# Optimization experiments

Measured on AMD Instinct MI355X. Metric: run time of the kernel, lower is better.

## Reference

```python
import jax, jax.numpy as jnp
import numpy as np
from jax import lax

DIM = 1024
H = 16          # num_heads
HD = DIM // H   # head dim (qk and v identical)
D_INNER = 4     # fast-weight inner dim
CHUNK = 16
BASE_LR = 1e-3
KSZ = 4         # short conv kernel size


def short_conv(x, w):
    # x: (b, l, c), w: (c, KSZ). Depthwise causal conv + residual (as in ShortConvolution).
    xT = jnp.transpose(x, (0, 2, 1))  # (b, c, l)
    y = lax.conv_general_dilated(xT, w[:, None, :], window_strides=(1,),
                                 padding=[(KSZ - 1, 0)], feature_group_count=x.shape[-1],
                                 dimension_numbers=('NCH', 'OIH', 'NCH'))
    return jnp.transpose(y + xT, (0, 2, 1))


def l2norm(x):
    # interpret torch.norm(..., dim=-1) as L2 normalization over head dim (required for shape consistency)
    return x / jnp.linalg.norm(x, axis=-1, keepdims=True)


def attn(q, k, v):
    # flash_attn_func equivalent: non-causal softmax attention, scale 1/sqrt(d)
    # q: (b, D, h, d), k/v: (b, L, h, d)
    s = jnp.einsum('bqhd,bkhd->bhqk', q, k) / jnp.sqrt(jnp.asarray(q.shape[-1], q.dtype))
    p = jax.nn.softmax(s, axis=-1)
    return jnp.einsum('bhqk,bkhd->bqhd', p, v)


def setup_inputs() -> dict:
    key = jax.random.key(0)
    ks = jax.random.split(key, 12)
    b, l = 4, 4096
    s = 1.0 / np.sqrt(DIM)
    return {
        'hidden_states': jax.random.normal(ks[0], (b, l, DIM), jnp.float32),
        'Wq': jax.random.normal(ks[1], (DIM, DIM), jnp.float32) * s,
        'Wk': jax.random.normal(ks[2], (DIM, DIM), jnp.float32) * s,
        'Wv': jax.random.normal(ks[3], (DIM, DIM), jnp.float32) * s,
        'Wlr': jax.random.normal(ks[4], (H * 2, DIM), jnp.float32) * s,
        'Wg': jax.random.normal(ks[5], (DIM, DIM), jnp.float32) * s,
        'Wo': jax.random.normal(ks[6], (DIM, DIM), jnp.float32) * s,
        'cq': jax.random.normal(ks[7], (DIM, KSZ), jnp.float32) * 0.1,
        'ck': jax.random.normal(ks[8], (DIM, KSZ), jnp.float32) * 0.1,
        'cv': jax.random.normal(ks[9], (DIM, KSZ), jnp.float32) * 0.1,
        'W_in_init': jax.random.normal(ks[10], (1, D_INNER, H, HD), jnp.float32) / np.sqrt(HD),
        'W_out_init': jax.random.normal(ks[11], (1, D_INNER, H, HD), jnp.float32) / np.sqrt(D_INNER),
        'ln_g': jnp.ones((HD,), jnp.float32),
        'ln_b': jnp.zeros((HD,), jnp.float32),
    }


def _forward(hidden_states, Wq, Wk, Wv, Wlr, Wg, Wo, cq, ck, cv, W_in_init, W_out_init, ln_g, ln_b):
    b, l, _ = hidden_states.shape
    q = l2norm(jax.nn.silu(short_conv(hidden_states @ Wq.T, cq)).reshape(b, l, H, HD))
    k = l2norm(jax.nn.silu(short_conv(hidden_states @ Wk.T, ck)).reshape(b, l, H, HD))
    v = jax.nn.silu(short_conv(hidden_states @ Wv.T, cv)).reshape(b, l, H, HD)
    lr = jax.nn.softplus(hidden_states @ Wlr.T + BASE_LR).reshape(b, l, H, 2)

    nc = l // CHUNK
    to_chunks = lambda x: x.reshape(b, nc, CHUNK, H, -1).transpose(1, 0, 2, 3, 4)
    qc, kc, vc, lrc = map(to_chunks, (q, k, v, lr))

    W_in0 = jnp.broadcast_to(W_in_init, (b, D_INNER, H, HD))
    W_out0 = jnp.broadcast_to(W_out_init, (b, D_INNER, H, HD))
    mask = jnp.tril(jnp.ones((CHUNK, CHUNK), jnp.float32))  # causal within chunk (diag kept)

    def step(carry, xs):
        W_in, W_out = carry
        q_t, k_t, v_t, lr_t = xs  # (b, CHUNK, H, d) / lr (b, CHUNK, H, 2)
        k_h = jax.nn.softmax(jnp.einsum('blhd,bDhd->blhD', k_t, W_in), axis=-1) * lr_t[..., 1:]
        q_h = jax.nn.softmax(jnp.einsum('blhd,bDhd->blhD', q_t, W_in), axis=-1)
        qk = jnp.einsum('bqhD,bkhD->bhqk', q_h, k_h) * mask
        o_t = jnp.einsum('bqhD,bDhd->bqhd', q_h, W_out) + jnp.einsum('bhqk,bkhd->bqhd', qk, v_t)
        W_out = W_out + jnp.einsum('bnhD,bnhd->bDhd', k_h, v_t)
        lr_in = lr_t[:, :1, :, 0:1]    # (b,1,h,1)
        lr_out = lr_t[:, :1, :, 1:2]
        # two nested test-time gradient steps via attention
        for _ in range(2):
            g_out = -attn(W_in, k_t, v_t)
            g_in = -attn(W_out, v_t, k_t)
            W_in = W_in - lr_in * g_in
            W_out = W_out - lr_out * g_out
        return (W_in, W_out), o_t

    _, o = lax.scan(step, (W_in0, W_out0), (qc, kc, vc, lrc))
    o = o.transpose(1, 0, 2, 3, 4).reshape(b, l, H, HD)

    mu = o.mean(-1, keepdims=True)
    var = ((o - mu) ** 2).mean(-1, keepdims=True)
    o = (o - mu) / jnp.sqrt(var + 1e-5) * ln_g + ln_b
    o = o.reshape(b, l, DIM)
    gate = hidden_states @ Wg.T
    return (o * gate) @ Wo.T


def reference(hidden_states, Wq, Wk, Wv, Wlr, Wg, Wo, cq, ck, cv, W_in_init, W_out_init, ln_g, ln_b):
    return _forward(hidden_states, Wq, Wk, Wv, Wlr, Wg, Wo, cq, ck, cv, W_in_init, W_out_init, ln_g, ln_b)
```

## Files before the change

### kernel.cpp

```cpp
#include <hip/hip_runtime.h>
#include <cstdint>
#include <cstddef>

#define DIM    1024
#define NH     16
#define HD     64
#define CHUNK_ 16
#define SEQ    4096
#define BATCH  4
#define NROWS  (BATCH * SEQ)
#define NCHUNK (SEQ / CHUNK_)
#define SEG    64
#define NSEG   (SEQ / SEG)

using bf16x8 = __attribute__((ext_vector_type(8))) short;
using f32x4  = __attribute__((ext_vector_type(4))) float;
typedef union { bf16x8 v; uint32_t u[4]; } B8;

#define MFMA16(a, b, c) __builtin_amdgcn_mfma_f32_16x16x32_bf16((a), (b), (c), 0, 0, 0)

__device__ __forceinline__ ushort f2bf(float f) {
    uint32_t u = __float_as_uint(f);
    u += 0x7FFFu + ((u >> 16) & 1u);
    return (ushort)(u >> 16);
}
__device__ __forceinline__ uint32_t pack2(float a, float b) {
    return (uint32_t)f2bf(a) | ((uint32_t)f2bf(b) << 16);
}
__device__ __forceinline__ float dot4(const float4 a, const float4 b) {
    return a.x*b.x + a.y*b.y + a.z*b.z + a.w*b.w;
}

template <int N>
__device__ __forceinline__ float ror16(float x) {
    return __int_as_float(__builtin_amdgcn_update_dpp(
        0, __float_as_int(x), 0x120 + N, 0xF, 0xF, true));
}
__device__ __forceinline__ float dppsum16(float x) {
    x += ror16<1>(x); x += ror16<2>(x);
    x += ror16<4>(x); x += ror16<8>(x);
    return x;
}

#define SYNC() do { asm volatile("" ::: "memory");          \
                    __builtin_amdgcn_wave_barrier();        \
                    __builtin_amdgcn_sched_barrier(0); } while (0)

__global__ __launch_bounds__(256)
void gemm_nt_bf16(const float* __restrict__ A, const float* __restrict__ B,
                  float* __restrict__ C, int K, int ldc)
{
    __shared__ ushort As[128][64];
    __shared__ ushort Bs[128][64];

    const int tid  = threadIdx.x;
    const int m0   = blockIdx.y * 128, n0 = blockIdx.x * 128;
    const int wave = tid >> 6, lane = tid & 63;
    const int wm   = (wave >> 1) * 64, wn = (wave & 1) * 64;
    const int frow = lane & 15, fkg = lane >> 4;
    const int srow = tid >> 1, shalf = tid & 1;

    f32x4 acc[4][4];
#pragma unroll
    for (int i = 0; i < 4; ++i)
#pragma unroll
        for (int j = 0; j < 4; ++j) acc[i][j] = (f32x4){0.f, 0.f, 0.f, 0.f};

    const float* Ap0 = A + (size_t)(m0 + srow) * K + shalf * 16;
    const float* Bp0 = B + (size_t)(n0 + srow) * K + shalf * 16;
    const int swz0 = ((shalf * 2 + 0) ^ (srow & 7)) * 8;
    const int swz1 = ((shalf * 2 + 1) ^ (srow & 7)) * 8;
    const int rsw  = (frow & 7);

    for (int kt = 0; kt < K; kt += 32) {
        float4 a0 = *(const float4*)(Ap0 + kt);
        float4 a1 = *(const float4*)(Ap0 + kt + 4);
        float4 a2 = *(const float4*)(Ap0 + kt + 8);
        float4 a3 = *(const float4*)(Ap0 + kt + 12);
        float4 b0 = *(const float4*)(Bp0 + kt);
        float4 b1 = *(const float4*)(Bp0 + kt + 4);
        float4 b2 = *(const float4*)(Bp0 + kt + 8);
        float4 b3 = *(const float4*)(Bp0 + kt + 12);

        __syncthreads();
        uint4 u;
        u.x = pack2(a0.x, a0.y); u.y = pack2(a0.z, a0.w);
        u.z = pack2(a1.x, a1.y); u.w = pack2(a1.z, a1.w);
        *(uint4*)&As[srow][swz0] = u;
        u.x = pack2(a2.x, a2.y); u.y = pack2(a2.z, a2.w);
        u.z = pack2(a3.x, a3.y); u.w = pack2(a3.z, a3.w);
        *(uint4*)&As[srow][swz1] = u;
        u.x = pack2(b0.x, b0.y); u.y = pack2(b0.z, b0.w);
        u.z = pack2(b1.x, b1.y); u.w = pack2(b1.z, b1.w);
        *(uint4*)&Bs[srow][swz0] = u;
        u.x = pack2(b2.x, b2.y); u.y = pack2(b2.z, b2.w);
        u.z = pack2(b3.x, b3.y); u.w = pack2(b3.z, b3.w);
        *(uint4*)&Bs[srow][swz1] = u;
        __syncthreads();

        bf16x8 af[4], bf[4];
#pragma unroll
        for (int i = 0; i < 4; ++i) {
            af[i] = *(const bf16x8*)&As[wm + i * 16 + frow][(fkg ^ rsw) * 8];
            bf[i] = *(const bf16x8*)&Bs[wn + i * 16 + frow][(fkg ^ rsw) * 8];
        }
#pragma unroll
        for (int mt = 0; mt < 4; ++mt)
#pragma unroll
            for (int nt = 0; nt < 4; ++nt)
                acc[mt][nt] = MFMA16(af[mt], bf[nt], acc[mt][nt]);
    }

    const int col = lane & 15, r4 = (lane >> 4) * 4;
#pragma unroll
    for (int mt = 0; mt < 4; ++mt)
#pragma unroll
        for (int nt = 0; nt < 4; ++nt)
#pragma unroll
            for (int j = 0; j < 4; ++j)
                C[(size_t)(m0 + wm + mt * 16 + r4 + j) * ldc +
                  (n0 + wn + nt * 16 + col)] = acc[mt][nt][j];
}

__global__ __launch_bounds__(256)
void lr_kernel(const float* __restrict__ hs, const float* __restrict__ Wlr,
               float* __restrict__ LR)
{
    __shared__ float row[DIM];
    const int r = blockIdx.x;
    const int t = threadIdx.x;
    *(float4*)&row[t * 4] = *(const float4*)&hs[(size_t)r * DIM + t * 4];
    __syncthreads();

    const int o = t >> 3;
    const int p = t & 7;
    const float* w = Wlr + (size_t)o * DIM + p * 128;
    const float* x = row + p * 128;
    float acc = 0.f;
#pragma unroll
    for (int i = 0; i < 32; ++i) {
        float4 xv = *(const float4*)(x + i * 4);
        float4 wv = *(const float4*)(w + i * 4);
        acc += dot4(xv, wv);
    }
    acc += __shfl_xor(acc, 1);
    acc += __shfl_xor(acc, 2);
    acc += __shfl_xor(acc, 4);
    if (p == 0) {
        float xx = acc + 0.001f;
        LR[(size_t)r * 32 + o] = (xx > 20.f) ? xx : log1pf(expf(xx));
    }
}

__global__ __launch_bounds__(256)
void halo_save(const float* __restrict__ Q, const float* __restrict__ K,
               const float* __restrict__ V, float* __restrict__ HALO)
{
    int idx = blockIdx.x;
    int tn  = idx / (BATCH * (NSEG - 1) * 3);
    int rem = idx - tn * (BATCH * (NSEG - 1) * 3);
    int b   = rem / ((NSEG - 1) * 3);
    int rem2= rem - b * ((NSEG - 1) * 3);
    int s   = rem2 / 3 + 1;
    int j   = rem2 - (s - 1) * 3;

    const float* buf = (tn == 0) ? Q : ((tn == 1) ? K : V);
    size_t src = ((size_t)(b * SEQ + s * SEG - 3 + j)) * DIM + threadIdx.x * 4;
    size_t dst = ((size_t)((tn * BATCH + b) * NSEG + s) * 3 + j) * DIM + threadIdx.x * 4;
    *(float4*)&HALO[dst] = *(const float4*)&buf[src];
}

__global__ __launch_bounds__(256)
void conv_inplace(float* __restrict__ Q, float* __restrict__ K,
                  float* __restrict__ V, const float* __restrict__ HALO,
                  const float* __restrict__ cq, const float* __restrict__ ck,
                  const float* __restrict__ cv)
{
    const int wid  = (blockIdx.x << 2) + (threadIdx.x >> 6);
    const int lane = threadIdx.x & 63;
    const int tn   = wid >> 12;
    const int rem  = wid & 4095;
    const int b    = rem >> 10;
    const int rem2 = rem & 1023;
    const int h    = rem2 >> 6;
    const int s    = rem2 & 63;
    const int c    = (h << 6) + lane;

    float* buf = (tn == 0) ? Q : ((tn == 1) ? K : V);
    const float* cw = (tn == 0) ? cq : ((tn == 1) ? ck : cv);
    float4 w4 = *(const float4*)(cw + (c << 2));

    float xm3 = 0.f, xm2 = 0.f, xm1 = 0.f;
    if (s > 0) {
        size_t hb = ((size_t)((tn * BATCH + b) * NSEG + s) * 3) * DIM + c;
        xm3 = HALO[hb];
        xm2 = HALO[hb + DIM];
        xm1 = HALO[hb + 2 * DIM];
    }

    size_t base = ((size_t)(b * SEQ + s * SEG)) * DIM + c;
    float x_next = buf[base];
#pragma unroll 4
    for (int i = 0; i < SEG; ++i) {
        float x = x_next;
        if (i < SEG - 1) x_next = buf[base + (size_t)(i + 1) * DIM];
        float y = xm3 * w4.x + xm2 * w4.y + xm1 * w4.z + x * w4.w + x;
        y = y / (1.f + __expf(-y));
        if (tn < 2) {
            float n2 = y * y;
#pragma unroll
            for (int m = 1; m < 64; m <<= 1) n2 += __shfl_xor(n2, m);
            y *= rsqrtf(n2);
        }
        buf[base + (size_t)i * DIM] = y;
        xm3 = xm2; xm2 = xm1; xm1 = x;
    }
}

__global__ __launch_bounds__(64)
void scan_kernel(const float* QP, const float* __restrict__ KP,
                 const float* __restrict__ VP, const float* __restrict__ LRb,
                 const float* __restrict__ GATE,
                 const float* __restrict__ Wi0, const float* __restrict__ Wo0,
                 const float* __restrict__ lng, const float* __restrict__ lnb,
                 float* OB)
{
    const int bh = blockIdx.x, b = bh >> 4, h = bh & 15;
    const int t  = threadIdx.x, lo = t & 15, g = t >> 4;

    __shared__ ushort KA[16][72], QA[16][72], VA[16][72];
    __shared__ ushort KT[64][24];
    __shared__ ushort VT[64][40];
    __shared__ ushort WiA[16][72], WoA[16][72];
    __shared__ ushort QKT[16][32];
    __shared__ ushort KH[16][32];
    __shared__ float  sG[16][68];

    for (int i = t; i < 16 * 72; i += 64) { ((ushort*)WiA)[i] = 0; ((ushort*)WoA)[i] = 0; }
    for (int i = t; i < 64 * 24; i += 64) ((ushort*)KT)[i] = 0;
    for (int i = t; i < 64 * 40; i += 64) ((ushort*)VT)[i] = 0;
    for (int i = t; i < 16 * 32; i += 64) { ((ushort*)QKT)[i] = 0; ((ushort*)KH)[i] = 0; }

    f32x4 wiC[4], woC[4];
#pragma unroll
    for (int n = 0; n < 4; ++n) { wiC[n] = (f32x4){0,0,0,0}; woC[n] = (f32x4){0,0,0,0}; }
    if (g == 0) {
#pragma unroll
        for (int n = 0; n < 4; ++n)
#pragma unroll
            for (int D = 0; D < 4; ++D) {
                float wi = Wi0[((size_t)D * NH + h) * HD + 16 * n + lo];
                float wo = Wo0[((size_t)D * NH + h) * HD + 16 * n + lo];
                wiC[n][D] = wi; woC[n][D] = wo;
                WiA[D][16 * n + lo] = f2bf(wi);
                WoA[D][16 * n + lo] = f2bf(wo);
                VT[16 * n + lo][16 + D] = f2bf(wo);
            }
    }
    SYNC();

    float lnGr[4], lnBr[4];
#pragma unroll
    for (int n = 0; n < 4; ++n) { lnGr[n] = lng[16 * n + lo]; lnBr[n] = lnb[16 * n + lo]; }

    const int rowb = b * SEQ;
    float4 pq[4], pk[4], pv[4], pg[4];
    float plr_q, plr_i, plr_o;
    {
#pragma unroll
        for (int i = 0; i < 4; ++i) {
            size_t go = (size_t)(rowb + i * 4 + g) * DIM + h * 64 + 4 * lo;
            pq[i] = *(const float4*)&QP[go];
            pk[i] = *(const float4*)&KP[go];
            pv[i] = *(const float4*)&VP[go];
            pg[i] = *(const float4*)&GATE[go];
        }
        plr_q = LRb[(size_t)(rowb + lo) * 32 + h * 2 + 1];
        plr_i = LRb[(size_t)rowb * 32 + h * 2];
        plr_o = LRb[(size_t)rowb * 32 + h * 2 + 1];
    }

    const f32x4 z4 = (f32x4){0.f, 0.f, 0.f, 0.f};
    const uint32_t pmsk = (g < 2) ? 0xFFFFFFFFu : 0u;
    const int L0 = (lo + 32 * g) & 63, L1 = (L0 + 16) & 63;

    for (int c = 0; c < NCHUNK; ++c) {
        const int rb = rowb + c * CHUNK_;

#pragma unroll
        for (int i = 0; i < 4; ++i) {
            const int row = i * 4 + g;
            *(float4*)&sG[row][4 * lo] = pg[i];
            uint2 uq; uq.x = pack2(pq[i].x, pq[i].y); uq.y = pack2(pq[i].z, pq[i].w);
            *(uint2*)&QA[row][4 * lo] = uq;
            uint2 uk; uk.x = pack2(pk[i].x, pk[i].y); uk.y = pack2(pk[i].z, pk[i].w);
            *(uint2*)&KA[row][4 * lo] = uk;
            uint2 uv; uv.x = pack2(pv[i].x, pv[i].y); uv.y = pack2(pv[i].z, pv[i].w);
            *(uint2*)&VA[row][4 * lo] = uv;
            KT[4 * lo + 0][row] = (ushort)(uk.x & 0xFFFF);
            KT[4 * lo + 1][row] = (ushort)(uk.x >> 16);
            KT[4 * lo + 2][row] = (ushort)(uk.y & 0xFFFF);
            KT[4 * lo + 3][row] = (ushort)(uk.y >> 16);
            VT[4 * lo + 0][row] = (ushort)(uv.x & 0xFFFF);
            VT[4 * lo + 1][row] = (ushort)(uv.x >> 16);
            VT[4 * lo + 2][row] = (ushort)(uv.y & 0xFFFF);
            VT[4 * lo + 3][row] = (ushort)(uv.y >> 16);
        }
        const float lr1    = plr_q;
        const float lr_in  = plr_i;
        const float lr_out = plr_o;

        if (c + 1 < NCHUNK) {
            const int rb2 = rb + CHUNK_;
#pragma unroll
            for (int i = 0; i < 4; ++i) {
                size_t go = (size_t)(rb2 + i * 4 + g) * DIM + h * 64 + 4 * lo;
                pq[i] = *(const float4*)&QP[go];
                pk[i] = *(const float4*)&KP[go];
                pv[i] = *(const float4*)&VP[go];
                pg[i] = *(const float4*)&GATE[go];
            }
            plr_q = LRb[(size_t)(rb2 + lo) * 32 + h * 2 + 1];
            plr_i = LRb[(size_t)rb2 * 32 + h * 2];
            plr_o = LRb[(size_t)rb2 * 32 + h * 2 + 1];
        }
        SYNC();

        bf16x8 xWi0 = *(const bf16x8*)&WiA[lo][g * 8];
        bf16x8 xWi1 = *(const bf16x8*)&WiA[lo][g * 8 + 32];
        f32x4 cK = MFMA16(xWi0, *(const bf16x8*)&KA[lo][g * 8], z4);
        cK = MFMA16(xWi1, *(const bf16x8*)&KA[lo][g * 8 + 32], cK);
        f32x4 cQ = MFMA16(xWi0, *(const bf16x8*)&QA[lo][g * 8], z4);
        cQ = MFMA16(xWi1, *(const bf16x8*)&QA[lo][g * 8 + 32], cQ);

        float mK = fmaxf(fmaxf(cK[0], cK[1]), fmaxf(cK[2], cK[3]));
        float ek0 = __expf(cK[0] - mK), ek1 = __expf(cK[1] - mK);
        float ek2 = __expf(cK[2] - mK), ek3 = __expf(cK[3] - mK);
        float ivk = lr1 / (ek0 + ek1 + ek2 + ek3);
        float kh0 = ek0 * ivk, kh1 = ek1 * ivk, kh2 = ek2 * ivk, kh3 = ek3 * ivk;

        float mQ = fmaxf(fmaxf(cQ[0], cQ[1]), fmaxf(cQ[2], cQ[3]));
        float eq0 = __expf(cQ[0] - mQ), eq1 = __expf(cQ[1] - mQ);
        float eq2 = __expf(cQ[2] - mQ), eq3 = __expf(cQ[3] - mQ);
        float ivq = 1.f / (eq0 + eq1 + eq2 + eq3);
        float qh0 = eq0 * ivq, qh1 = eq1 * ivq, qh2 = eq2 * ivq, qh3 = eq3 * ivq;

        B8 aQh, bKh;
        aQh.u[0] = aQh.u[1] = aQh.u[2] = aQh.u[3] = 0;
        bKh.u[0] = bKh.u[1] = bKh.u[2] = bKh.u[3] = 0;
        if (g == 0) {
            aQh.u[0] = pack2(qh0, qh1); aQh.u[1] = pack2(qh2, qh3);
            bKh.u[0] = pack2(kh0, kh1); bKh.u[1] = pack2(kh2, kh3);
        }
        f32x4 cQK = MFMA16(aQh.v, bKh.v, z4);

#pragma unroll
        for (int r = 0; r < 4; ++r) {
            const int q = 4 * g + r;
            QKT[q][lo] = (lo <= q) ? f2bf(cQK[r]) : (ushort)0;
        }
        if (g == 0) {
            QKT[lo][16] = f2bf(qh0); QKT[lo][17] = f2bf(qh1);
            QKT[lo][18] = f2bf(qh2); QKT[lo][19] = f2bf(qh3);
            KH[0][lo] = f2bf(kh0); KH[1][lo] = f2bf(kh1);
            KH[2][lo] = f2bf(kh2); KH[3][lo] = f2bf(kh3);
        }
        SYNC();

        bf16x8 aO = *(const bf16x8*)&QKT[lo][g * 8];
        f32x4 oA[4];
#pragma unroll
        for (int n = 0; n < 4; ++n)
            oA[n] = MFMA16(aO, *(const bf16x8*)&VT[16 * n + lo][g * 8], z4);
#pragma unroll
        for (int r = 0; r < 4; ++r) {
            float s1 = oA[0][r] + oA[1][r] + oA[2][r] + oA[3][r];
            float s2 = oA[0][r] * oA[0][r] + oA[1][r] * oA[1][r] +
                       oA[2][r] * oA[2][r] + oA[3][r] * oA[3][r];
            s1 = dppsum16(s1); s2 = dppsum16(s2);
            float mu = s1 * (1.f / 64.f);
            float rstd = rsqrtf(s2 * (1.f / 64.f) - mu * mu + 1e-5f);
            const int q = 4 * g + r;
#pragma unroll
            for (int n = 0; n < 4; ++n) {
                float val = (oA[n][r] - mu) * rstd * lnGr[n] + lnBr[n];
                val *= sG[q][16 * n + lo];
                OB[(size_t)(rb + q) * DIM + h * 64 + 16 * n + lo] = val;
            }
        }
        {
            bf16x8 aKH = *(const bf16x8*)&KH[lo][g * 8];
#pragma unroll
            for (int n = 0; n < 4; ++n)
                woC[n] = MFMA16(aKH, *(const bf16x8*)&VT[16 * n + lo][g * 8], woC[n]);
        }
        if (g == 0) {
#pragma unroll
            for (int n = 0; n < 4; ++n)
#pragma unroll
                for (int D = 0; D < 4; ++D)
                    WoA[D][16 * n + lo] = f2bf(woC[n][D]);
        }
        SYNC();

#pragma unroll
        for (int it = 0; it < 2; ++it) {
            bf16x8 aK0 = *(const bf16x8*)&KA[lo][g * 8];
            bf16x8 aK1 = *(const bf16x8*)&KA[lo][g * 8 + 32];
            bf16x8 aV0 = *(const bf16x8*)&VA[lo][g * 8];
            bf16x8 aV1 = *(const bf16x8*)&VA[lo][g * 8 + 32];
            bf16x8 bWi0 = *(const bf16x8*)&WiA[lo][g * 8];
            bf16x8 bWi1 = *(const bf16x8*)&WiA[lo][g * 8 + 32];
            bf16x8 bWo0 = *(const bf16x8*)&WoA[lo][g * 8];
            bf16x8 bWo1 = *(const bf16x8*)&WoA[lo][g * 8 + 32];
            f32x4 s0T = MFMA16(aK0, bWi0, z4);
            s0T = MFMA16(aK1, bWi1, s0T);
            f32x4 s1T = MFMA16(aV0, bWo0, z4);
            s1T = MFMA16(aV1, bWo1, s1T);

            float x0[4], x1[4];
#pragma unroll
            for (int r = 0; r < 4; ++r) {
                x0[r] = s0T[r] * 0.125f;
                x1[r] = s1T[r] * 0.125f;
            }
            float m0 = fmaxf(fmaxf(x0[0], x0[1]), fmaxf(x0[2], x0[3]));
            float m1 = fmaxf(fmaxf(x1[0], x1[1]), fmaxf(x1[2], x1[3]));
            m0 = fmaxf(m0, __shfl_xor(m0, 16)); m0 = fmaxf(m0, __shfl_xor(m0, 32));
            m1 = fmaxf(m1, __shfl_xor(m1, 16)); m1 = fmaxf(m1, __shfl_xor(m1, 32));
            float e0[4], e1[4];
#pragma unroll
            for (int r = 0; r < 4; ++r) {
                e0[r] = __expf(x0[r] - m0);
                e1[r] = __expf(x1[r] - m1);
            }
            float su0 = e0[0] + e0[1] + e0[2] + e0[3];
            float su1 = e1[0] + e1[1] + e1[2] + e1[3];
            su0 += __shfl_xor(su0, 16); su0 += __shfl_xor(su0, 32);
            su1 += __shfl_xor(su1, 16); su1 += __shfl_xor(su1, 32);
            const float w0 = lr_out / su0;
            const float w1 = lr_in / su1;

            uint32_t p00 = pack2(e0[0] * w0, e0[1] * w0);
            uint32_t p01 = pack2(e0[2] * w0, e0[3] * w0);
            uint32_t p10 = pack2(e1[0] * w1, e1[1] * w1);
            uint32_t p11 = pack2(e1[2] * w1, e1[3] * w1);
            B8 aP0, aP1;
            aP0.u[0] = (uint32_t)__shfl((int)p00, L0) & pmsk;
            aP0.u[1] = (uint32_t)__shfl((int)p01, L0) & pmsk;
            aP0.u[2] = (uint32_t)__shfl((int)p00, L1) & pmsk;
            aP0.u[3] = (uint32_t)__shfl((int)p01, L1) & pmsk;
            aP1.u[0] = (uint32_t)__shfl((int)p10, L0) & pmsk;
            aP1.u[1] = (uint32_t)__shfl((int)p11, L0) & pmsk;
            aP1.u[2] = (uint32_t)__shfl((int)p10, L1) & pmsk;
            aP1.u[3] = (uint32_t)__shfl((int)p11, L1) & pmsk;

#pragma unroll
            for (int n = 0; n < 4; ++n) {
                woC[n] = MFMA16(aP0.v, *(const bf16x8*)&VT[16 * n + lo][g * 8], woC[n]);
                wiC[n] = MFMA16(aP1.v, *(const bf16x8*)&KT[16 * n + lo][g * 8], wiC[n]);
            }
            if (g == 0) {
#pragma unroll
                for (int n = 0; n < 4; ++n)
#pragma unroll
                    for (int D = 0; D < 4; ++D) {
                        WiA[D][16 * n + lo] = f2bf(wiC[n][D]);
                        WoA[D][16 * n + lo] = f2bf(woC[n][D]);
                        if (it == 1) VT[16 * n + lo][16 + D] = f2bf(woC[n][D]);
                    }
            }
            SYNC();
        }
    }
}

extern "C" void kernel_launch(void* const* d_in, const int* in_sizes, int n_in,
                              void* d_out, int out_size, void* d_ws, size_t ws_size,
                              hipStream_t stream)
{
    const float* hs  = (const float*)d_in[0];
    const float* Wq  = (const float*)d_in[1];
    const float* Wk  = (const float*)d_in[2];
    const float* Wv  = (const float*)d_in[3];
    const float* Wlr = (const float*)d_in[4];
    const float* Wg  = (const float*)d_in[5];
    const float* Wo  = (const float*)d_in[6];
    const float* cq  = (const float*)d_in[7];
    const float* ck  = (const float*)d_in[8];
    const float* cv  = (const float*)d_in[9];
    const float* Wi0 = (const float*)d_in[10];
    const float* Wo0 = (const float*)d_in[11];
    const float* lng = (const float*)d_in[12];
    const float* lnb = (const float*)d_in[13];

    float* ws   = (float*)d_ws;
    float* Q    = ws;
    float* K    = Q + (size_t)NROWS * DIM;
    float* V    = K + (size_t)NROWS * DIM;
    float* LRb  = V + (size_t)NROWS * DIM;
    float* HALO = LRb + (size_t)NROWS * 32;
    float* GATE = (float*)d_out;
    float* OBUF = Q;

    dim3 blk(256);

    gemm_nt_bf16<<<dim3(8, 128), blk, 0, stream>>>(hs, Wq, Q,    1024, DIM);
    gemm_nt_bf16<<<dim3(8, 128), blk, 0, stream>>>(hs, Wk, K,    1024, DIM);
    gemm_nt_bf16<<<dim3(8, 128), blk, 0, stream>>>(hs, Wv, V,    1024, DIM);
    gemm_nt_bf16<<<dim3(8, 128), blk, 0, stream>>>(hs, Wg, GATE, 1024, DIM);

    lr_kernel<<<NROWS, blk, 0, stream>>>(hs, Wlr, LRb);

    halo_save<<<3 * BATCH * (NSEG - 1) * 3, blk, 0, stream>>>(Q, K, V, HALO);
    conv_inplace<<<(3 * BATCH * NH * NSEG) / 4, blk, 0, stream>>>(Q, K, V, HALO,
                                                                  cq, ck, cv);

    scan_kernel<<<BATCH * NH, dim3(64), 0, stream>>>(Q, K, V, LRb, GATE,
                                                     Wi0, Wo0, lng, lnb, OBUF);

    gemm_nt_bf16<<<dim3(8, 128), blk, 0, stream>>>(OBUF, Wo, (float*)d_out,
                                                   1024, 1024);
}
```

Before: 2.051 ms.

## Store intermediates in bf16, use direct-to-LDS GEMM loads, double-buffer scan staging

Inputs and weights are converted to bf16 up front, and a new GEMM loads tiles straight into LDS with global_load_lds over a 64-wide K step. Q/K/V, the conv halo and the scan output now live in bf16, which halves the memory traffic of the conv, scan and output GEMM. The scan kernel double-buffers its LDS staging so the next chunk is written during the last gradient iteration, removing one wave barrier per chunk. The cost is extra conversion passes, more rounding in the intermediates, and the serial scan may still dominate the runtime.

```diff
diff --git a/kernel.cpp b/kernel.cpp
--- a/kernel.cpp
+++ b/kernel.cpp
@@ -27,6 +27,9 @@
 __device__ __forceinline__ uint32_t pack2(float a, float b) {
     return (uint32_t)f2bf(a) | ((uint32_t)f2bf(b) << 16);
 }
+__device__ __forceinline__ float b2f(ushort u) {
+    return __uint_as_float(((uint32_t)u) << 16);
+}
 __device__ __forceinline__ float dot4(const float4 a, const float4 b) {
     return a.x*b.x + a.y*b.y + a.z*b.z + a.w*b.w;
 }
@@ -46,80 +49,95 @@
                     __builtin_amdgcn_wave_barrier();        \
                     __builtin_amdgcn_sched_barrier(0); } while (0)
 
+__device__ __forceinline__ void gl_lds16(const void* g, void* l) {
+    __builtin_amdgcn_global_load_lds(
+        (const __attribute__((address_space(1))) void*)g,
+        (__attribute__((address_space(3))) void*)l, 16, 0, 0);
+}
+
 __global__ __launch_bounds__(256)
-void gemm_nt_bf16(const float* __restrict__ A, const float* __restrict__ B,
-                  float* __restrict__ C, int K, int ldc)
-{
-    __shared__ ushort As[128][64];
-    __shared__ ushort Bs[128][64];
-
-    const int tid  = threadIdx.x;
-    const int m0   = blockIdx.y * 128, n0 = blockIdx.x * 128;
-    const int wave = tid >> 6, lane = tid & 63;
-    const int wm   = (wave >> 1) * 64, wn = (wave & 1) * 64;
-    const int frow = lane & 15, fkg = lane >> 4;
-    const int srow = tid >> 1, shalf = tid & 1;
-
-    f32x4 acc[4][4];
-#pragma unroll
-    for (int i = 0; i < 4; ++i)
-#pragma unroll
-        for (int j = 0; j < 4; ++j) acc[i][j] = (f32x4){0.f, 0.f, 0.f, 0.f};
-
-    const float* Ap0 = A + (size_t)(m0 + srow) * K + shalf * 16;
-    const float* Bp0 = B + (size_t)(n0 + srow) * K + shalf * 16;
-    const int swz0 = ((shalf * 2 + 0) ^ (srow & 7)) * 8;
-    const int swz1 = ((shalf * 2 + 1) ^ (srow & 7)) * 8;
-    const int rsw  = (frow & 7);
-
-    for (int kt = 0; kt < K; kt += 32) {
-        float4 a0 = *(const float4*)(Ap0 + kt);
-        float4 a1 = *(const float4*)(Ap0 + kt + 4);
-        float4 a2 = *(const float4*)(Ap0 + kt + 8);
-        float4 a3 = *(const float4*)(Ap0 + kt + 12);
-        float4 b0 = *(const float4*)(Bp0 + kt);
-        float4 b1 = *(const float4*)(Bp0 + kt + 4);
-        float4 b2 = *(const float4*)(Bp0 + kt + 8);
-        float4 b3 = *(const float4*)(Bp0 + kt + 12);
-
-        __syncthreads();
+void f2b_kernel(const float* __restrict__ in, ushort* __restrict__ out, int n8)
+{
+    int i = blockIdx.x * 256 + threadIdx.x;
+    const int stride = gridDim.x * 256;
+    for (; i < n8; i += stride) {
+        float4 a = *(const float4*)&in[(size_t)i * 8];
+        float4 b = *(const float4*)&in[(size_t)i * 8 + 4];
         uint4 u;
-        u.x = pack2(a0.x, a0.y); u.y = pack2(a0.z, a0.w);
-        u.z = pack2(a1.x, a1.y); u.w = pack2(a1.z, a1.w);
-        *(uint4*)&As[srow][swz0] = u;
-        u.x = pack2(a2.x, a2.y); u.y = pack2(a2.z, a2.w);
-        u.z = pack2(a3.x, a3.y); u.w = pack2(a3.z, a3.w);
-        *(uint4*)&As[srow][swz1] = u;
-        u.x = pack2(b0.x, b0.y); u.y = pack2(b0.z, b0.w);
-        u.z = pack2(b1.x, b1.y); u.w = pack2(b1.z, b1.w);
-        *(uint4*)&Bs[srow][swz0] = u;
-        u.x = pack2(b2.x, b2.y); u.y = pack2(b2.z, b2.w);
-        u.z = pack2(b3.x, b3.y); u.w = pack2(b3.z, b3.w);
-        *(uint4*)&Bs[srow][swz1] = u;
-        __syncthreads();
-
-        bf16x8 af[4], bf[4];
-#pragma unroll
-        for (int i = 0; i < 4; ++i) {
-            af[i] = *(const bf16x8*)&As[wm + i * 16 + frow][(fkg ^ rsw) * 8];
-            bf[i] = *(const bf16x8*)&Bs[wn + i * 16 + frow][(fkg ^ rsw) * 8];
-        }
-#pragma unroll
-        for (int mt = 0; mt < 4; ++mt)
-#pragma unroll
-            for (int nt = 0; nt < 4; ++nt)
-                acc[mt][nt] = MFMA16(af[mt], bf[nt], acc[mt][nt]);
-    }
-
-    const int col = lane & 15, r4 = (lane >> 4) * 4;
-#pragma unroll
-    for (int mt = 0; mt < 4; ++mt)
-#pragma unroll
-        for (int nt = 0; nt < 4; ++nt)
-#pragma unroll
-            for (int j = 0; j < 4; ++j)
-                C[(size_t)(m0 + wm + mt * 16 + r4 + j) * ldc +
-                  (n0 + wn + nt * 16 + col)] = acc[mt][nt][j];
+        u.x = pack2(a.x, a.y); u.y = pack2(a.z, a.w);
+        u.z = pack2(b.x, b.y); u.w = pack2(b.z, b.w);
+        *(uint4*)&out[(size_t)i * 8] = u;
+    }
+}
+
+#define GEMM_LDS_BODY(EPILOG)                                                  \
+    __shared__ ushort As[128][64];                                             \
+    __shared__ ushort Bs[128][64];                                             \
+    const int tid  = threadIdx.x, wave = tid >> 6, lane = tid & 63;            \
+    const int m0   = blockIdx.y * 128, n0 = blockIdx.x * 128;                  \
+    const int lo   = lane & 15, kg = lane >> 4;                                \
+    const int wm   = (wave >> 1) * 64, wn = (wave & 1) * 64;                   \
+    const int rin  = lane >> 3, sl = lane & 7;                                 \
+    const int sb   = 32 * wave;                                                \
+    f32x4 acc[4][4];                                                           \
+    _Pragma("unroll")                                                          \
+    for (int i = 0; i < 4; ++i)                                                \
+        _Pragma("unroll")                                                      \
+        for (int j = 0; j < 4; ++j) acc[i][j] = (f32x4){0.f, 0.f, 0.f, 0.f};   \
+    const int swz = lo & 7;                                                    \
+    for (int kt = 0; kt < K; kt += 64) {                                       \
+        __syncthreads();                                                       \
+        _Pragma("unroll")                                                      \
+        for (int i = 0; i < 4; ++i) {                                          \
+            const int row = sb + 8 * i + rin;                                  \
+            const int gs  = sl ^ (row & 7);                                    \
+            gl_lds16(A + (size_t)(m0 + row) * K + kt + gs * 8,                 \
+                     &As[sb + 8 * i][0]);                                      \
+            gl_lds16(B + (size_t)(n0 + row) * K + kt + gs * 8,                 \
+                     &Bs[sb + 8 * i][0]);                                      \
+        }                                                                      \
+        __syncthreads();                                                       \
+        bf16x8 af[2][4], bfr[2][4];                                            \
+        _Pragma("unroll")                                                      \
+        for (int kk = 0; kk < 2; ++kk)                                         \
+            _Pragma("unroll")                                                  \
+            for (int m = 0; m < 4; ++m) {                                      \
+                const int s = (kk * 4 + kg) ^ swz;                             \
+                af[kk][m]  = *(const bf16x8*)&As[wm + m * 16 + lo][s * 8];     \
+                bfr[kk][m] = *(const bf16x8*)&Bs[wn + m * 16 + lo][s * 8];     \
+            }                                                                  \
+        _Pragma("unroll")                                                      \
+        for (int kk = 0; kk < 2; ++kk)                                         \
+            _Pragma("unroll")                                                  \
+            for (int mt = 0; mt < 4; ++mt)                                     \
+                _Pragma("unroll")                                              \
+                for (int nt = 0; nt < 4; ++nt)                                 \
+                    acc[mt][nt] = MFMA16(af[kk][mt], bfr[kk][nt], acc[mt][nt]);\
+    }                                                                          \
+    const int col = lane & 15, r4 = (lane >> 4) * 4;                           \
+    _Pragma("unroll")                                                          \
+    for (int mt = 0; mt < 4; ++mt)                                             \
+        _Pragma("unroll")                                                      \
+        for (int nt = 0; nt < 4; ++nt)                                         \
+            _Pragma("unroll")                                                  \
+            for (int j = 0; j < 4; ++j) {                                      \
+                size_t idx = (size_t)(m0 + wm + mt * 16 + r4 + j) * DIM +      \
+                             n0 + wn + nt * 16 + col;                          \
+                EPILOG;                                                        \
+            }
+
+__global__ __launch_bounds__(256)
+void gemm_lds_b16o(const ushort* __restrict__ A, const ushort* __restrict__ B,
+                   ushort* __restrict__ C, int K)
+{
+    GEMM_LDS_BODY(C[idx] = f2bf(acc[mt][nt][j]))
+}
+
+__global__ __launch_bounds__(256)
+void gemm_lds_f32o(const ushort* __restrict__ A, const ushort* __restrict__ B,
+                   float* __restrict__ C, int K)
+{
+    GEMM_LDS_BODY(C[idx] = acc[mt][nt][j])
 }
 
 __global__ __launch_bounds__(256)
@@ -153,8 +171,8 @@
 }
 
 __global__ __launch_bounds__(256)
-void halo_save(const float* __restrict__ Q, const float* __restrict__ K,
-               const float* __restrict__ V, float* __restrict__ HALO)
+void halo_save(const ushort* __restrict__ Q, const ushort* __restrict__ K,
+               const ushort* __restrict__ V, ushort* __restrict__ HALO)
 {
     int idx = blockIdx.x;
     int tn  = idx / (BATCH * (NSEG - 1) * 3);
@@ -164,15 +182,15 @@
     int s   = rem2 / 3 + 1;
     int j   = rem2 - (s - 1) * 3;
 
-    const float* buf = (tn == 0) ? Q : ((tn == 1) ? K : V);
+    const ushort* buf = (tn == 0) ? Q : ((tn == 1) ? K : V);
     size_t src = ((size_t)(b * SEQ + s * SEG - 3 + j)) * DIM + threadIdx.x * 4;
     size_t dst = ((size_t)((tn * BATCH + b) * NSEG + s) * 3 + j) * DIM + threadIdx.x * 4;
-    *(float4*)&HALO[dst] = *(const float4*)&buf[src];
+    *(uint2*)&HALO[dst] = *(const uint2*)&buf[src];
 }
 
 __global__ __launch_bounds__(256)
-void conv_inplace(float* __restrict__ Q, float* __restrict__ K,
-                  float* __restrict__ V, const float* __restrict__ HALO,
+void conv_inplace(ushort* __restrict__ Q, ushort* __restrict__ K,
+                  ushort* __restrict__ V, const ushort* __restrict__ HALO,
                   const float* __restrict__ cq, const float* __restrict__ ck,
                   const float* __restrict__ cv)
 {
@@ -186,24 +204,24 @@
     const int s    = rem2 & 63;
     const int c    = (h << 6) + lane;
 
-    float* buf = (tn == 0) ? Q : ((tn == 1) ? K : V);
+    ushort* buf = (tn == 0) ? Q : ((tn == 1) ? K : V);
     const float* cw = (tn == 0) ? cq : ((tn == 1) ? ck : cv);
     float4 w4 = *(const float4*)(cw + (c << 2));
 
     float xm3 = 0.f, xm2 = 0.f, xm1 = 0.f;
     if (s > 0) {
         size_t hb = ((size_t)((tn * BATCH + b) * NSEG + s) * 3) * DIM + c;
-        xm3 = HALO[hb];
-        xm2 = HALO[hb + DIM];
-        xm1 = HALO[hb + 2 * DIM];
+        xm3 = b2f(HALO[hb]);
+        xm2 = b2f(HALO[hb + DIM]);
+        xm1 = b2f(HALO[hb + 2 * DIM]);
     }
 
     size_t base = ((size_t)(b * SEQ + s * SEG)) * DIM + c;
-    float x_next = buf[base];
+    float x_next = b2f(buf[base]);
 #pragma unroll 4
     for (int i = 0; i < SEG; ++i) {
         float x = x_next;
-        if (i < SEG - 1) x_next = buf[base + (size_t)(i + 1) * DIM];
+        if (i < SEG - 1) x_next = b2f(buf[base + (size_t)(i + 1) * DIM]);
         float y = xm3 * w4.x + xm2 * w4.y + xm1 * w4.z + x * w4.w + x;
         y = y / (1.f + __expf(-y));
         if (tn < 2) {
@@ -212,33 +230,32 @@
             for (int m = 1; m < 64; m <<= 1) n2 += __shfl_xor(n2, m);
             y *= rsqrtf(n2);
         }
-        buf[base + (size_t)i * DIM] = y;
+        buf[base + (size_t)i * DIM] = f2bf(y);
         xm3 = xm2; xm2 = xm1; xm1 = x;
     }
 }
 
 __global__ __launch_bounds__(64)
-void scan_kernel(const float* QP, const float* __restrict__ KP,
-                 const float* __restrict__ VP, const float* __restrict__ LRb,
+void scan_kernel(const ushort* QP, const ushort* __restrict__ KP,
+                 const ushort* __restrict__ VP, const float* __restrict__ LRb,
                  const float* __restrict__ GATE,
                  const float* __restrict__ Wi0, const float* __restrict__ Wo0,
                  const float* __restrict__ lng, const float* __restrict__ lnb,
-                 float* OB)
+                 ushort* OB)
 {
     const int bh = blockIdx.x, b = bh >> 4, h = bh & 15;
     const int t  = threadIdx.x, lo = t & 15, g = t >> 4;
 
-    __shared__ ushort KA[16][72], QA[16][72], VA[16][72];
-    __shared__ ushort KT[64][24];
-    __shared__ ushort VT[64][40];
+    __shared__ ushort KA2[2][16][72], QA2[2][16][72], VA2[2][16][72];
+    __shared__ float  sG2[2][16][68];
+    __shared__ ushort KT2[2][64][24];
+    __shared__ ushort VT2[2][64][40];
     __shared__ ushort WiA[16][72], WoA[16][72];
-    __shared__ ushort QKT[16][32];
-    __shared__ ushort KH[16][32];
-    __shared__ float  sG[16][68];
+    __shared__ ushort QKT[16][32], KH[16][32];
 
     for (int i = t; i < 16 * 72; i += 64) { ((ushort*)WiA)[i] = 0; ((ushort*)WoA)[i] = 0; }
-    for (int i = t; i < 64 * 24; i += 64) ((ushort*)KT)[i] = 0;
-    for (int i = t; i < 64 * 40; i += 64) ((ushort*)VT)[i] = 0;
+    for (int i = t; i < 2 * 64 * 24; i += 64) ((ushort*)KT2)[i] = 0;
+    for (int i = t; i < 2 * 64 * 40; i += 64) ((ushort*)VT2)[i] = 0;
     for (int i = t; i < 16 * 32; i += 64) { ((ushort*)QKT)[i] = 0; ((ushort*)KH)[i] = 0; }
 
     f32x4 wiC[4], woC[4];
@@ -254,7 +271,7 @@
                 wiC[n][D] = wi; woC[n][D] = wo;
                 WiA[D][16 * n + lo] = f2bf(wi);
                 WoA[D][16 * n + lo] = f2bf(wo);
-                VT[16 * n + lo][16 + D] = f2bf(wo);
+                VT2[0][16 * n + lo][16 + D] = f2bf(wo);
             }
     }
     SYNC();
@@ -264,48 +281,67 @@
     for (int n = 0; n < 4; ++n) { lnGr[n] = lng[16 * n + lo]; lnBr[n] = lnb[16 * n + lo]; }
 
     const int rowb = b * SEQ;
-    float4 pq[4], pk[4], pv[4], pg[4];
+    const ushort* QPh = QP + h * 64;
+    const ushort* KPh = KP + h * 64;
+    const ushort* VPh = VP + h * 64;
+    const float*  GPh = GATE + h * 64;
+    ushort*       OBh = OB + h * 64;
+
+    uint2 pq[4], pk[4], pv[4];
+    float4 pg[4];
     float plr_q, plr_i, plr_o;
+
     {
 #pragma unroll
         for (int i = 0; i < 4; ++i) {
-            size_t go = (size_t)(rowb + i * 4 + g) * DIM + h * 64 + 4 * lo;
-            pq[i] = *(const float4*)&QP[go];
-            pk[i] = *(const float4*)&KP[go];
-            pv[i] = *(const float4*)&VP[go];
-            pg[i] = *(const float4*)&GATE[go];
+            size_t go = (size_t)(rowb + i * 4 + g) * DIM + 4 * lo;
+            pq[i] = *(const uint2*)&QPh[go];
+            pk[i] = *(const uint2*)&KPh[go];
+            pv[i] = *(const uint2*)&VPh[go];
+            pg[i] = *(const float4*)&GPh[go];
         }
         plr_q = LRb[(size_t)(rowb + lo) * 32 + h * 2 + 1];
         plr_i = LRb[(size_t)rowb * 32 + h * 2];
         plr_o = LRb[(size_t)rowb * 32 + h * 2 + 1];
     }
 
+    auto STAGE = [&](int nb) {
+#pragma unroll
+        for (int i = 0; i < 4; ++i) {
+            const int row = i * 4 + g;
+            *(float4*)&sG2[nb][row][4 * lo] = pg[i];
+            *(uint2*)&QA2[nb][row][4 * lo] = pq[i];
+            *(uint2*)&KA2[nb][row][4 * lo] = pk[i];
+            *(uint2*)&VA2[nb][row][4 * lo] = pv[i];
+            uint2 uk = pk[i], uv = pv[i];
+            KT2[nb][4 * lo + 0][row] = (ushort)(uk.x & 0xFFFF);
+            KT2[nb][4 * lo + 1][row] = (ushort)(uk.x >> 16);
+            KT2[nb][4 * lo + 2][row] = (ushort)(uk.y & 0xFFFF);
+            KT2[nb][4 * lo + 3][row] = (ushort)(uk.y >> 16);
+            VT2[nb][4 * lo + 0][row] = (ushort)(uv.x & 0xFFFF);
+            VT2[nb][4 * lo + 1][row] = (ushort)(uv.x >> 16);
+            VT2[nb][4 * lo + 2][row] = (ushort)(uv.y & 0xFFFF);
+            VT2[nb][4 * lo + 3][row] = (ushort)(uv.y >> 16);
+        }
+    };
+
+    STAGE(0);
+    SYNC();
+
     const f32x4 z4 = (f32x4){0.f, 0.f, 0.f, 0.f};
     const uint32_t pmsk = (g < 2) ? 0xFFFFFFFFu : 0u;
     const int L0 = (lo + 32 * g) & 63, L1 = (L0 + 16) & 63;
 
     for (int c = 0; c < NCHUNK; ++c) {
-        const int rb = rowb + c * CHUNK_;
-
-#pragma unroll
-        for (int i = 0; i < 4; ++i) {
-            const int row = i * 4 + g;
-            *(float4*)&sG[row][4 * lo] = pg[i];
-            uint2 uq; uq.x = pack2(pq[i].x, pq[i].y); uq.y = pack2(pq[i].z, pq[i].w);
-            *(uint2*)&QA[row][4 * lo] = uq;
-            uint2 uk; uk.x = pack2(pk[i].x, pk[i].y); uk.y = pack2(pk[i].z, pk[i].w);
-            *(uint2*)&KA[row][4 * lo] = uk;
-            uint2 uv; uv.x = pack2(pv[i].x, pv[i].y); uv.y = pack2(pv[i].z, pv[i].w);
-            *(uint2*)&VA[row][4 * lo] = uv;
-            KT[4 * lo + 0][row] = (ushort)(uk.x & 0xFFFF);
-            KT[4 * lo + 1][row] = (ushort)(uk.x >> 16);
-            KT[4 * lo + 2][row] = (ushort)(uk.y & 0xFFFF);
-            KT[4 * lo + 3][row] = (ushort)(uk.y >> 16);
-            VT[4 * lo + 0][row] = (ushort)(uv.x & 0xFFFF);
-            VT[4 * lo + 1][row] = (ushort)(uv.x >> 16);
-            VT[4 * lo + 2][row] = (ushort)(uv.y & 0xFFFF);
-            VT[4 * lo + 3][row] = (ushort)(uv.y >> 16);
-        }
+        const int rb  = rowb + c * CHUNK_;
+        const int cur = c & 1, nxt = cur ^ 1;
+        ushort (*KAc)[72] = KA2[cur];
+        ushort (*QAc)[72] = QA2[cur];
+        ushort (*VAc)[72] = VA2[cur];
+        float  (*sGc)[68] = sG2[cur];
+        ushort (*KTc)[24] = KT2[cur];
+        ushort (*VTc)[40] = VT2[cur];
+
         const float lr1    = plr_q;
         const float lr_in  = plr_i;
         const float lr_out = plr_o;
@@ -314,24 +350,23 @@
             const int rb2 = rb + CHUNK_;
 #pragma unroll
             for (int i = 0; i < 4; ++i) {
-                size_t go = (size_t)(rb2 + i * 4 + g) * DIM + h * 64 + 4 * lo;
-                pq[i] = *(const float4*)&QP[go];
-                pk[i] = *(const float4*)&KP[go];
-                pv[i] = *(const float4*)&VP[go];
-                pg[i] = *(const float4*)&GATE[go];
+                size_t go = (size_t)(rb2 + i * 4 + g) * DIM + 4 * lo;
+                pq[i] = *(const uint2*)&QPh[go];
+                pk[i] = *(const uint2*)&KPh[go];
+                pv[i] = *(const uint2*)&VPh[go];
+                pg[i] = *(const float4*)&GPh[go];
             }
             plr_q = LRb[(size_t)(rb2 + lo) * 32 + h * 2 + 1];
             plr_i = LRb[(size_t)rb2 * 32 + h * 2];
             plr_o = LRb[(size_t)rb2 * 32 + h * 2 + 1];
         }
-        SYNC();
 
         bf16x8 xWi0 = *(const bf16x8*)&WiA[lo][g * 8];
         bf16x8 xWi1 = *(const bf16x8*)&WiA[lo][g * 8 + 32];
-        f32x4 cK = MFMA16(xWi0, *(const bf16x8*)&KA[lo][g * 8], z4);
-        cK = MFMA16(xWi1, *(const bf16x8*)&KA[lo][g * 8 + 32], cK);
-        f32x4 cQ = MFMA16(xWi0, *(const bf16x8*)&QA[lo][g * 8], z4);
-        cQ = MFMA16(xWi1, *(const bf16x8*)&QA[lo][g * 8 + 32], cQ);
+        f32x4 cK = MFMA16(xWi0, *(const bf16x8*)&KAc[lo][g * 8], z4);
+        cK = MFMA16(xWi1, *(const bf16x8*)&KAc[lo][g * 8 + 32], cK);
+        f32x4 cQ = MFMA16(xWi0, *(const bf16x8*)&QAc[lo][g * 8], z4);
+        cQ = MFMA16(xWi1, *(const bf16x8*)&QAc[lo][g * 8 + 32], cQ);
 
         float mK = fmaxf(fmaxf(cK[0], cK[1]), fmaxf(cK[2], cK[3]));
         float ek0 = __expf(cK[0] - mK), ek1 = __expf(cK[1] - mK);
@@ -371,7 +406,7 @@
         f32x4 oA[4];
 #pragma unroll
         for (int n = 0; n < 4; ++n)
-            oA[n] = MFMA16(aO, *(const bf16x8*)&VT[16 * n + lo][g * 8], z4);
+            oA[n] = MFMA16(aO, *(const bf16x8*)&VTc[16 * n + lo][g * 8], z4);
 #pragma unroll
         for (int r = 0; r < 4; ++r) {
             float s1 = oA[0][r] + oA[1][r] + oA[2][r] + oA[3][r];
@@ -384,15 +419,15 @@
 #pragma unroll
             for (int n = 0; n < 4; ++n) {
                 float val = (oA[n][r] - mu) * rstd * lnGr[n] + lnBr[n];
-                val *= sG[q][16 * n + lo];
-                OB[(size_t)(rb + q) * DIM + h * 64 + 16 * n + lo] = val;
+                val *= sGc[q][16 * n + lo];
+                OBh[(size_t)(rb + q) * DIM + 16 * n + lo] = f2bf(val);
             }
         }
         {
             bf16x8 aKH = *(const bf16x8*)&KH[lo][g * 8];
 #pragma unroll
             for (int n = 0; n < 4; ++n)
-                woC[n] = MFMA16(aKH, *(const bf16x8*)&VT[16 * n + lo][g * 8], woC[n]);
+                woC[n] = MFMA16(aKH, *(const bf16x8*)&VTc[16 * n + lo][g * 8], woC[n]);
         }
         if (g == 0) {
 #pragma unroll
@@ -405,10 +440,10 @@
 
 #pragma unroll
         for (int it = 0; it < 2; ++it) {
-            bf16x8 aK0 = *(const bf16x8*)&KA[lo][g * 8];
-            bf16x8 aK1 = *(const bf16x8*)&KA[lo][g * 8 + 32];
-            bf16x8 aV0 = *(const bf16x8*)&VA[lo][g * 8];
-            bf16x8 aV1 = *(const bf16x8*)&VA[lo][g * 8 + 32];
+            bf16x8 aK0 = *(const bf16x8*)&KAc[lo][g * 8];
+            bf16x8 aK1 = *(const bf16x8*)&KAc[lo][g * 8 + 32];
+            bf16x8 aV0 = *(const bf16x8*)&VAc[lo][g * 8];
+            bf16x8 aV1 = *(const bf16x8*)&VAc[lo][g * 8 + 32];
             bf16x8 bWi0 = *(const bf16x8*)&WiA[lo][g * 8];
             bf16x8 bWi1 = *(const bf16x8*)&WiA[lo][g * 8 + 32];
             bf16x8 bWo0 = *(const bf16x8*)&WoA[lo][g * 8];
@@ -457,9 +492,12 @@
 
 #pragma unroll
             for (int n = 0; n < 4; ++n) {
-                woC[n] = MFMA16(aP0.v, *(const bf16x8*)&VT[16 * n + lo][g * 8], woC[n]);
-                wiC[n] = MFMA16(aP1.v, *(const bf16x8*)&KT[16 * n + lo][g * 8], wiC[n]);
-            }
+                woC[n] = MFMA16(aP0.v, *(const bf16x8*)&VTc[16 * n + lo][g * 8], woC[n]);
+                wiC[n] = MFMA16(aP1.v, *(const bf16x8*)&KTc[16 * n + lo][g * 8], wiC[n]);
+            }
+
+            if (it == 1 && c + 1 < NCHUNK) STAGE(nxt);
+
             if (g == 0) {
 #pragma unroll
                 for (int n = 0; n < 4; ++n)
@@ -467,7 +505,7 @@
                     for (int D = 0; D < 4; ++D) {
                         WiA[D][16 * n + lo] = f2bf(wiC[n][D]);
                         WoA[D][16 * n + lo] = f2bf(woC[n][D]);
-                        if (it == 1) VT[16 * n + lo][16 + D] = f2bf(woC[n][D]);
+                        if (it == 1) VT2[nxt][16 * n + lo][16 + D] = f2bf(woC[n][D]);
                     }
             }
             SYNC();
@@ -494,31 +532,42 @@
     const float* lng = (const float*)d_in[12];
     const float* lnb = (const float*)d_in[13];
 
-    float* ws   = (float*)d_ws;
-    float* Q    = ws;
-    float* K    = Q + (size_t)NROWS * DIM;
-    float* V    = K + (size_t)NROWS * DIM;
-    float* LRb  = V + (size_t)NROWS * DIM;
-    float* HALO = LRb + (size_t)NROWS * 32;
-    float* GATE = (float*)d_out;
-    float* OBUF = Q;
+    ushort* Qb   = (ushort*)d_ws;
+    ushort* Kb   = Qb + (size_t)NROWS * DIM;
+    ushort* Vb   = Kb + (size_t)NROWS * DIM;
+    ushort* hsb  = Vb + (size_t)NROWS * DIM;
+    ushort* Wqb  = hsb + (size_t)NROWS * DIM;
+    ushort* Wkb  = Wqb + (size_t)DIM * DIM;
+    ushort* Wvb  = Wkb + (size_t)DIM * DIM;
+    ushort* Wgb  = Wvb + (size_t)DIM * DIM;
+    ushort* Wob  = Wgb + (size_t)DIM * DIM;
+    ushort* HALO = Wob + (size_t)DIM * DIM;
+    float*  LRb  = (float*)(HALO + (size_t)3 * BATCH * NSEG * 3 * DIM);
+    float*  GATE = (float*)d_out;
+    ushort* OBUF = hsb;
 
     dim3 blk(256);
 
-    gemm_nt_bf16<<<dim3(8, 128), blk, 0, stream>>>(hs, Wq, Q,    1024, DIM);
-    gemm_nt_bf16<<<dim3(8, 128), blk, 0, stream>>>(hs, Wk, K,    1024, DIM);
-    gemm_nt_bf16<<<dim3(8, 128), blk, 0, stream>>>(hs, Wv, V,    1024, DIM);
-    gemm_nt_bf16<<<dim3(8, 128), blk, 0, stream>>>(hs, Wg, GATE, 1024, DIM);
+    f2b_kernel<<<2048, blk, 0, stream>>>(hs, hsb, NROWS * DIM / 8);
+    f2b_kernel<<<512, blk, 0, stream>>>(Wq, Wqb, DIM * DIM / 8);
+    f2b_kernel<<<512, blk, 0, stream>>>(Wk, Wkb, DIM * DIM / 8);
+    f2b_kernel<<<512, blk, 0, stream>>>(Wv, Wvb, DIM * DIM / 8);
+    f2b_kernel<<<512, blk, 0, stream>>>(Wg, Wgb, DIM * DIM / 8);
+    f2b_kernel<<<512, blk, 0, stream>>>(Wo, Wob, DIM * DIM / 8);
+
+    gemm_lds_b16o<<<dim3(8, 128), blk, 0, stream>>>(hsb, Wqb, Qb, 1024);
+    gemm_lds_b16o<<<dim3(8, 128), blk, 0, stream>>>(hsb, Wkb, Kb, 1024);
+    gemm_lds_b16o<<<dim3(8, 128), blk, 0, stream>>>(hsb, Wvb, Vb, 1024);
+    gemm_lds_f32o<<<dim3(8, 128), blk, 0, stream>>>(hsb, Wgb, GATE, 1024);
 
     lr_kernel<<<NROWS, blk, 0, stream>>>(hs, Wlr, LRb);
 
-    halo_save<<<3 * BATCH * (NSEG - 1) * 3, blk, 0, stream>>>(Q, K, V, HALO);
-    conv_inplace<<<(3 * BATCH * NH * NSEG) / 4, blk, 0, stream>>>(Q, K, V, HALO,
+    halo_save<<<3 * BATCH * (NSEG - 1) * 3, blk, 0, stream>>>(Qb, Kb, Vb, HALO);
+    conv_inplace<<<(3 * BATCH * NH * NSEG) / 4, blk, 0, stream>>>(Qb, Kb, Vb, HALO,
                                                                   cq, ck, cv);
 
-    scan_kernel<<<BATCH * NH, dim3(64), 0, stream>>>(Q, K, V, LRb, GATE,
+    scan_kernel<<<BATCH * NH, dim3(64), 0, stream>>>(Qb, Kb, Vb, LRb, GATE,
                                                      Wi0, Wo0, lng, lnb, OBUF);
 
-    gemm_nt_bf16<<<dim3(8, 128), blk, 0, stream>>>(OBUF, Wo, (float*)d_out,
-                                                   1024, 1024);
-}
+    gemm_lds_f32o<<<dim3(8, 128), blk, 0, stream>>>(OBUF, Wob, (float*)d_out, 1024);
+}
```

After: 1.751 ms. 14.6% less time.
